# Optimization experiments

Measured on AMD Instinct MI355X. Metric: run time of the kernel, lower is better.

## Reference

```python
import jax, jax.numpy as jnp
import numpy as np


def setup_inputs() -> dict:
    key = jax.random.key(0)
    k0, k1, k2, k3 = jax.random.split(key, 4)
    B, S, D, F, E = 2, 2048, 1024, 4096, 8
    hidden_states = jax.random.normal(k0, (B, S, D), dtype=jnp.float32)
    Wr = jax.random.normal(k1, (E, D), dtype=jnp.float32) * 0.02   # router Linear weight [E, D]
    W1 = jax.random.normal(k2, (E, D, F), dtype=jnp.float32) * 0.02  # expert w1 (transposed torch layout)
    W2 = jax.random.normal(k3, (E, F, D), dtype=jnp.float32) * 0.02  # expert w2
    return {"hidden_states": hidden_states, "Wr": Wr, "W1": W1, "W2": W2, "top_k": 2}


def reference(hidden_states, Wr, W1, W2, top_k):
    # hidden_states: [B, S, D]; Wr: [E, D]; W1: [E, D, F]; W2: [E, F, D]
    E = Wr.shape[0]
    dt = hidden_states.dtype

    # Router: logits -> top-k expert indices. NOTE: the original module computes
    # softmax routing weights over the top-k logits but never applies them in the
    # combine step, so the output is an UNWEIGHTED sum over selected experts.
    router_logits = jnp.einsum('bsd,ed->bse', hidden_states, Wr)
    _, topk_idx = jax.lax.top_k(router_logits, top_k)            # [B, S, K]

    # mask[b,s,e] = 1 if expert e is in token (b,s)'s top-k (indices are distinct)
    mask = (jax.nn.one_hot(topk_idx, E, dtype=dt).sum(axis=-2) > 0).astype(dt)  # [B, S, E]

    # Dense per-expert FFN (SiLU MLP, no bias, dropout=identity in eval):
    h = jax.nn.silu(jnp.einsum('bsd,edf->bsef', hidden_states, W1))  # [B, S, E, F]
    y = jnp.einsum('bsef,efd->bsed', h, W2)                          # [B, S, E, D]

    # Combine: unweighted sum over selected experts (faithful to source)
    return jnp.einsum('bsed,bse->bsd', y, mask)
```

## Files before the change

kernel.cpp:

```cpp
#include <hip/hip_runtime.h>
#include <hip/hip_bf16.h>
#include <stdint.h>

#define TOKENS 4096
#define DDIM 1024
#define FDIM 4096
#define NEXP 8
#define BM 128
#define BN 128
#define BK2 32

typedef __attribute__((ext_vector_type(4))) float f32x4;
typedef __attribute__((ext_vector_type(8))) short short8;

__device__ __forceinline__ unsigned short f2bf(float f) {
    union { float f; uint32_t u; } v; v.f = f;
    uint32_t u = v.u;
    return (unsigned short)((u + 0x7fff + ((u >> 16) & 1)) >> 16);
}

#define BARRIER() asm volatile("s_barrier" ::: "memory")
#define WAIT_VM0() asm volatile("s_waitcnt vmcnt(0)" ::: "memory")
#define WAIT_VM4() asm volatile("s_waitcnt vmcnt(4)" ::: "memory")
#define WAIT_LGKM0() asm volatile("s_waitcnt lgkmcnt(0)" ::: "memory")
#define GLDS(SRC, DST) __builtin_amdgcn_global_load_lds( \
    (const __attribute__((address_space(1))) void*)(SRC), \
    (__attribute__((address_space(3))) void*)(DST), 16, 0, 0)

__device__ __forceinline__ short8 dsr(uint32_t addr) {
    short8 d;
    asm volatile("ds_read_b128 %0, %1" : "=v"(d) : "v"(addr));
    return d;
}

__global__ __launch_bounds__(256) void cvt_x(const float* __restrict__ x,
                                             unsigned short* __restrict__ xb, int n) {
    int i = (blockIdx.x * 256 + threadIdx.x) * 8;
    if (i >= n) return;
    float4 a = *(const float4*)(x + i);
    float4 b = *(const float4*)(x + i + 4);
    short8 o;
    o[0] = f2bf(a.x); o[1] = f2bf(a.y); o[2] = f2bf(a.z); o[3] = f2bf(a.w);
    o[4] = f2bf(b.x); o[5] = f2bf(b.y); o[6] = f2bf(b.z); o[7] = f2bf(b.w);
    *(short8*)(xb + i) = o;
}

__global__ __launch_bounds__(256) void transpose_cvt(const float* __restrict__ in,
                                                     unsigned short* __restrict__ out,
                                                     int R, int C) {
    __shared__ float tile[32][33];
    int e = blockIdx.z;
    int r0 = blockIdx.y * 32, c0 = blockIdx.x * 32;
    const float* src = in + (size_t)e * R * C;
    unsigned short* dst = out + (size_t)e * R * C;
    int t = threadIdx.x;
    int rr = t >> 3;
    int cc = (t & 7) * 4;
    float4 v = *(const float4*)(src + (size_t)(r0 + rr) * C + c0 + cc);
    tile[rr][cc + 0] = v.x; tile[rr][cc + 1] = v.y;
    tile[rr][cc + 2] = v.z; tile[rr][cc + 3] = v.w;
    __syncthreads();
    int oc = rr;
    int orr = cc;
    ushort4 o;
    o.x = f2bf(tile[orr + 0][oc]);
    o.y = f2bf(tile[orr + 1][oc]);
    o.z = f2bf(tile[orr + 2][oc]);
    o.w = f2bf(tile[orr + 3][oc]);
    *(ushort4*)(dst + (size_t)(c0 + oc) * R + r0 + orr) = o;
}

__global__ __launch_bounds__(256) void router(const float* __restrict__ x,
                                              const float* __restrict__ wr,
                                              int* __restrict__ cnt,
                                              int* __restrict__ list) {
    __shared__ float wl[NEXP * DDIM];
    int t = threadIdx.x;
    for (int i = t; i < NEXP * DDIM; i += 256) wl[i] = wr[i];
    __syncthreads();
    int tok = blockIdx.x * 4 + (t >> 6);
    int lane = t & 63;
    float acc[NEXP];
#pragma unroll
    for (int e = 0; e < NEXP; e++) acc[e] = 0.f;
    const float* xr = x + (size_t)tok * DDIM;
    for (int d = lane; d < DDIM; d += 64) {
        float xv = xr[d];
#pragma unroll
        for (int e = 0; e < NEXP; e++) acc[e] += xv * wl[e * DDIM + d];
    }
#pragma unroll
    for (int e = 0; e < NEXP; e++) {
#pragma unroll
        for (int off = 32; off; off >>= 1) acc[e] += __shfl_xor(acc[e], off);
    }
    if (lane == 0) {
        int e1 = 0; float v1 = acc[0];
        for (int e = 1; e < NEXP; e++) if (acc[e] > v1) { v1 = acc[e]; e1 = e; }
        int e2 = -1; float v2 = -1e30f;
        for (int e = 0; e < NEXP; e++) if (e != e1 && acc[e] > v2) { v2 = acc[e]; e2 = e; }
        int p1 = atomicAdd(&cnt[e1], 1);
        list[e1 * TOKENS + p1] = tok;
        int p2 = atomicAdd(&cnt[e2], 1);
        list[e2 * TOKENS + p2] = tok;
    }
}

__global__ void setup(const int* __restrict__ cnt, int* __restrict__ off,
                      int* __restrict__ wbA, int* __restrict__ wbB,
                      int* __restrict__ qctr) {
    if (threadIdx.x == 0) {
        int s = 0, ta = 0, tb = 0;
        for (int e = 0; e < NEXP; e++) {
            off[e] = s; s += cnt[e];
            wbA[e] = ta; wbB[e] = tb;
            int ntm = (cnt[e] + BM - 1) / BM;
            ta += ntm * (FDIM / BN);
            tb += ntm * (DDIM / BN) * 2;
        }
        wbA[NEXP] = ta; wbB[NEXP] = tb;
        qctr[0] = 0; qctr[1] = 0;
    }
}

template <bool GATHER_A, bool SILU, int KSPLIT>
__global__ __launch_bounds__(256, 3) void gemm_moe8(
    const unsigned short* __restrict__ Abase,
    const unsigned short* __restrict__ Wt,
    const int* __restrict__ cnt, const int* __restrict__ off,
    const int* __restrict__ list,
    const int* __restrict__ wbase,
    int* __restrict__ qctr,
    unsigned short* __restrict__ Hout,
    float* __restrict__ Yout,
    int KD, int KLEN, int NW) {
    __shared__ alignas(16) unsigned short As[3][BM * BK2];
    __shared__ alignas(16) unsigned short Bs[3][BN * BK2];
    __shared__ int wsh;

    const int t = threadIdx.x;
    const int lane = t & 63;
    const int wid = t >> 6;
    const int wm = wid >> 1, wn = wid & 1;
    const int r16 = lane & 15, g = lane >> 4;
    const int total = wbase[NEXP];

    const uint32_t asB = (uint32_t)(uintptr_t)&As[0][0];
    const uint32_t bsB = (uint32_t)(uintptr_t)&Bs[0][0];
    uint32_t aAdr[4], bAdr[4];
#pragma unroll
    for (int mi = 0; mi < 4; mi++) {
        int row = wm * 64 + mi * 16 + r16;
        aAdr[mi] = asB + row * 64 + ((g ^ ((row >> 1) & 3)) << 4);
    }
#pragma unroll
    for (int nj = 0; nj < 4; nj++) {
        int row = wn * 64 + nj * 16 + r16;
        bAdr[nj] = bsB + row * 64 + ((g ^ ((row >> 1) & 3)) << 4);
    }

    for (;;) {
        if (t == 0) wsh = atomicAdd(qctr, 1);
        __syncthreads();
        int w = wsh;
        if (w >= total) break;

        int e = 0;
        while (e < NEXP - 1 && w >= wbase[e + 1]) e++;
        w -= wbase[e];
        const int n_e = cnt[e];
        const int ntm = (n_e + BM - 1) >> 7;
        int idx = w / ntm;
        const int mtile = w - idx * ntm;
        int kc = 0;
        if (KSPLIT == 2) { kc = idx & 1; idx >>= 1; }
        const int m0 = mtile * BM;
        const int n0 = idx * BN;
        const int base = off[e];
        const int k0 = kc * KLEN;

        const unsigned short* pA[2];
        const unsigned short* pB[2];
        int ldsOff[2];
#pragma unroll
        for (int i = 0; i < 2; i++) {
            int c = i * 256 + t;
            int row = c >> 2, p = c & 3;
            int cg = p ^ ((row >> 1) & 3);
            int arow = m0 + row; if (arow >= n_e) arow = n_e - 1;
            size_t grow = GATHER_A ? (size_t)list[e * TOKENS + arow] : (size_t)(base + arow);
            pA[i] = Abase + grow * (size_t)KD + k0 + (cg << 3);
            pB[i] = Wt + ((size_t)e * NW + n0 + row) * (size_t)KD + k0 + (cg << 3);
            ldsOff[i] = c * 16;
        }

        f32x4 acc[4][4];
#pragma unroll
        for (int i = 0; i < 4; i++)
#pragma unroll
            for (int j = 0; j < 4; j++) acc[i][j] = f32x4{0.f, 0.f, 0.f, 0.f};

#pragma unroll
        for (int s = 0; s < 2; ++s) {
#pragma unroll
            for (int i = 0; i < 2; i++) { GLDS(pA[i], (char*)As[s] + ldsOff[i]); pA[i] += BK2; }
#pragma unroll
            for (int i = 0; i < 2; i++) { GLDS(pB[i], (char*)Bs[s] + ldsOff[i]); pB[i] += BK2; }
        }
        WAIT_VM4();
        BARRIER();

        uint32_t o0 = 0, o1 = 8192, o2 = 16384;

        const int NT = KLEN / BK2;
        for (int tk = 0; tk < NT; ++tk) {
            if (tk + 2 < NT) {
#pragma unroll
                for (int i = 0; i < 2; i++) { GLDS(pA[i], (char*)As[0] + o2 + ldsOff[i]); pA[i] += BK2; }
#pragma unroll
                for (int i = 0; i < 2; i++) { GLDS(pB[i], (char*)Bs[0] + o2 + ldsOff[i]); pB[i] += BK2; }
            }

            short8 a0 = dsr(aAdr[0] + o0);
            short8 a1 = dsr(aAdr[1] + o0);
            short8 a2 = dsr(aAdr[2] + o0);
            short8 a3 = dsr(aAdr[3] + o0);
            short8 b0 = dsr(bAdr[0] + o0);
            short8 b1 = dsr(bAdr[1] + o0);
            short8 b2 = dsr(bAdr[2] + o0);
            short8 b3 = dsr(bAdr[3] + o0);
            WAIT_LGKM0();
            __builtin_amdgcn_sched_barrier(0);

            __builtin_amdgcn_s_setprio(1);
            acc[0][0] = __builtin_amdgcn_mfma_f32_16x16x32_bf16(a0, b0, acc[0][0], 0, 0, 0);
            acc[0][1] = __builtin_amdgcn_mfma_f32_16x16x32_bf16(a0, b1, acc[0][1], 0, 0, 0);
            acc[0][2] = __builtin_amdgcn_mfma_f32_16x16x32_bf16(a0, b2, acc[0][2], 0, 0, 0);
            acc[0][3] = __builtin_amdgcn_mfma_f32_16x16x32_bf16(a0, b3, acc[0][3], 0, 0, 0);
            acc[1][0] = __builtin_amdgcn_mfma_f32_16x16x32_bf16(a1, b0, acc[1][0], 0, 0, 0);
            acc[1][1] = __builtin_amdgcn_mfma_f32_16x16x32_bf16(a1, b1, acc[1][1], 0, 0, 0);
            acc[1][2] = __builtin_amdgcn_mfma_f32_16x16x32_bf16(a1, b2, acc[1][2], 0, 0, 0);
            acc[1][3] = __builtin_amdgcn_mfma_f32_16x16x32_bf16(a1, b3, acc[1][3], 0, 0, 0);
            acc[2][0] = __builtin_amdgcn_mfma_f32_16x16x32_bf16(a2, b0, acc[2][0], 0, 0, 0);
            acc[2][1] = __builtin_amdgcn_mfma_f32_16x16x32_bf16(a2, b1, acc[2][1], 0, 0, 0);
            acc[2][2] = __builtin_amdgcn_mfma_f32_16x16x32_bf16(a2, b2, acc[2][2], 0, 0, 0);
            acc[2][3] = __builtin_amdgcn_mfma_f32_16x16x32_bf16(a2, b3, acc[2][3], 0, 0, 0);
            acc[3][0] = __builtin_amdgcn_mfma_f32_16x16x32_bf16(a3, b0, acc[3][0], 0, 0, 0);
            acc[3][1] = __builtin_amdgcn_mfma_f32_16x16x32_bf16(a3, b1, acc[3][1], 0, 0, 0);
            acc[3][2] = __builtin_amdgcn_mfma_f32_16x16x32_bf16(a3, b2, acc[3][2], 0, 0, 0);
            acc[3][3] = __builtin_amdgcn_mfma_f32_16x16x32_bf16(a3, b3, acc[3][3], 0, 0, 0);
            __builtin_amdgcn_s_setprio(0);

            if (tk + 1 < NT) {
                if (tk + 2 < NT) WAIT_VM4();
                else             WAIT_VM0();
                BARRIER();
            }
            uint32_t tmp = o0; o0 = o1; o1 = o2; o2 = tmp;
        }

#pragma unroll
        for (int mi = 0; mi < 4; ++mi) {
#pragma unroll
            for (int nj = 0; nj < 4; ++nj) {
#pragma unroll
                for (int qq = 0; qq < 4; ++qq) {
                    int lr = wm * 64 + mi * 16 + g * 4 + qq;
                    if (m0 + lr < n_e) {
                        int col = n0 + wn * 64 + nj * 16 + r16;
                        float v = acc[mi][nj][qq];
                        if (SILU) {
                            v = v / (1.f + __expf(-v));
                            Hout[(size_t)(base + m0 + lr) * NW + col] = f2bf(v);
                        } else {
                            int tok = list[e * TOKENS + m0 + lr];
                            atomicAdd(&Yout[(size_t)tok * NW + col], v);
                        }
                    }
                }
            }
        }
    }
}

extern "C" void kernel_launch(void* const* d_in, const int* in_sizes, int n_in,
                              void* d_out, int out_size, void* d_ws, size_t ws_size,
                              hipStream_t stream) {
    const float* X  = (const float*)d_in[0];
    const float* Wr = (const float*)d_in[1];
    const float* W1 = (const float*)d_in[2];
    const float* W2 = (const float*)d_in[3];
    float* Y = (float*)d_out;

    char* ws = (char*)d_ws;
    int* cnt  = (int*)(ws + 0);
    int* off  = (int*)(ws + 64);
    int* wbA  = (int*)(ws + 128);
    int* wbB  = (int*)(ws + 192);
    int* qctr = (int*)(ws + 256);
    int* list = (int*)(ws + 1024);
    unsigned short* Xb = (unsigned short*)(ws + (1ull << 20));
    unsigned short* WT = (unsigned short*)(ws + (16ull << 20));
    unsigned short* H  = (unsigned short*)(ws + (80ull << 20));

    hipMemsetAsync(d_out, 0, (size_t)out_size * sizeof(float), stream);
    hipMemsetAsync(cnt, 0, 32, stream);

    cvt_x<<<TOKENS * DDIM / (256 * 8), 256, 0, stream>>>(X, Xb, TOKENS * DDIM);
    router<<<TOKENS / 4, 256, 0, stream>>>(X, Wr, cnt, list);
    setup<<<1, 64, 0, stream>>>(cnt, off, wbA, wbB, qctr);

    transpose_cvt<<<dim3(FDIM / 32, DDIM / 32, NEXP), 256, 0, stream>>>(W1, WT, DDIM, FDIM);
    gemm_moe8<true, true, 1><<<768, 256, 0, stream>>>(
        Xb, WT, cnt, off, list, wbA, qctr + 0, H, nullptr, DDIM, DDIM, FDIM);

    transpose_cvt<<<dim3(DDIM / 32, FDIM / 32, NEXP), 256, 0, stream>>>(W2, WT, FDIM, DDIM);
    gemm_moe8<false, false, 2><<<768, 256, 0, stream>>>(
        H, WT, cnt, off, list, wbB, qctr + 1, nullptr, Y, FDIM, FDIM / 2, DDIM);
}
```

Baseline: 463.1 us.

## Partition persistent GEMM work queue per XCD with work stealing

Replaces the single global atomic work counter with eight per-XCD queues, each owning a contiguous slice of the tile range. Workgroups read their XCD id from a hardware register and pull from their own queue first, falling back to the other queues once it is drained. The goal is to keep neighbouring tiles, which share weight and activation panels, on the same XCD so its L2 is reused, and to spread atomic contention across eight counters. When its own queue is empty a workgroup may issue up to eight atomics before finding work, and the per-queue limits now have to be kept in step with the tile ordering.

New measurement: 1.227 ms. 165% more time.

```diff
diff --git a/kernel.cpp b/kernel.cpp
--- a/kernel.cpp
+++ b/kernel.cpp
@@ -108,7 +108,8 @@
 
 __global__ void setup(const int* __restrict__ cnt, int* __restrict__ off,
                       int* __restrict__ wbA, int* __restrict__ wbB,
-                      int* __restrict__ qctr) {
+                      int* __restrict__ qA, int* __restrict__ qlA,
+                      int* __restrict__ qB, int* __restrict__ qlB) {
     if (threadIdx.x == 0) {
         int s = 0, ta = 0, tb = 0;
         for (int e = 0; e < NEXP; e++) {
@@ -119,18 +120,23 @@
             tb += ntm * (DDIM / BN) * 2;
         }
         wbA[NEXP] = ta; wbB[NEXP] = tb;
-        qctr[0] = 0; qctr[1] = 0;
+        for (int x = 0; x < 8; x++) {
+            qA[x]  = (int)((long)ta * x / 8);
+            qlA[x] = (int)((long)ta * (x + 1) / 8);
+            qB[x]  = (int)((long)tb * x / 8);
+            qlB[x] = (int)((long)tb * (x + 1) / 8);
+        }
     }
 }
 
 template <bool GATHER_A, bool SILU, int KSPLIT>
-__global__ __launch_bounds__(256, 3) void gemm_moe8(
+__global__ __launch_bounds__(256, 3) void gemm_moe9(
     const unsigned short* __restrict__ Abase,
     const unsigned short* __restrict__ Wt,
     const int* __restrict__ cnt, const int* __restrict__ off,
     const int* __restrict__ list,
     const int* __restrict__ wbase,
-    int* __restrict__ qctr,
+    int* __restrict__ qctr, const int* __restrict__ qlim,
     unsigned short* __restrict__ Hout,
     float* __restrict__ Yout,
     int KD, int KLEN, int NW) {
@@ -143,7 +149,10 @@
     const int wid = t >> 6;
     const int wm = wid >> 1, wn = wid & 1;
     const int r16 = lane & 15, g = lane >> 4;
-    const int total = wbase[NEXP];
+
+    uint32_t xcd;
+    asm volatile("s_getreg_b32 %0, hwreg(HW_REG_XCC_ID)" : "=s"(xcd));
+    int myq = (int)(xcd & 7);
 
     const uint32_t asB = (uint32_t)(uintptr_t)&As[0][0];
     const uint32_t bsB = (uint32_t)(uintptr_t)&Bs[0][0];
@@ -160,10 +169,18 @@
     }
 
     for (;;) {
-        if (t == 0) wsh = atomicAdd(qctr, 1);
+        if (t == 0) {
+            int w = -1;
+            for (int k = 0; k < 8 && w < 0; k++) {
+                int q = (myq + k) & 7;
+                int cand = atomicAdd(&qctr[q], 1);
+                if (cand < qlim[q]) { w = cand; myq = q; }
+            }
+            wsh = w;
+        }
         __syncthreads();
         int w = wsh;
-        if (w >= total) break;
+        if (w < 0) break;
 
         int e = 0;
         while (e < NEXP - 1 && w >= wbase[e + 1]) e++;
@@ -297,7 +314,10 @@
     int* off  = (int*)(ws + 64);
     int* wbA  = (int*)(ws + 128);
     int* wbB  = (int*)(ws + 192);
-    int* qctr = (int*)(ws + 256);
+    int* qA   = (int*)(ws + 256);
+    int* qlA  = (int*)(ws + 288);
+    int* qB   = (int*)(ws + 320);
+    int* qlB  = (int*)(ws + 352);
     int* list = (int*)(ws + 1024);
     unsigned short* Xb = (unsigned short*)(ws + (1ull << 20));
     unsigned short* WT = (unsigned short*)(ws + (16ull << 20));
@@ -308,13 +328,13 @@
 
     cvt_x<<<TOKENS * DDIM / (256 * 8), 256, 0, stream>>>(X, Xb, TOKENS * DDIM);
     router<<<TOKENS / 4, 256, 0, stream>>>(X, Wr, cnt, list);
-    setup<<<1, 64, 0, stream>>>(cnt, off, wbA, wbB, qctr);
+    setup<<<1, 64, 0, stream>>>(cnt, off, wbA, wbB, qA, qlA, qB, qlB);
 
     transpose_cvt<<<dim3(FDIM / 32, DDIM / 32, NEXP), 256, 0, stream>>>(W1, WT, DDIM, FDIM);
-    gemm_moe8<true, true, 1><<<768, 256, 0, stream>>>(
-        Xb, WT, cnt, off, list, wbA, qctr + 0, H, nullptr, DDIM, DDIM, FDIM);
+    gemm_moe9<true, true, 1><<<768, 256, 0, stream>>>(
+        Xb, WT, cnt, off, list, wbA, qA, qlA, H, nullptr, DDIM, DDIM, FDIM);
 
     transpose_cvt<<<dim3(DDIM / 32, FDIM / 32, NEXP), 256, 0, stream>>>(W2, WT, FDIM, DDIM);
-    gemm_moe8<false, false, 2><<<768, 256, 0, stream>>>(
-        H, WT, cnt, off, list, wbB, qctr + 1, nullptr, Y, FDIM, FDIM / 2, DDIM);
-}
+    gemm_moe9<false, false, 2><<<768, 256, 0, stream>>>(
+        H, WT, cnt, off, list, wbB, qB, qlB, nullptr, Y, FDIM, FDIM / 2, DDIM);
+}
```

## Use 256x64 tiles with 8-wave blocks and 4-way K split in down-proj

Applied to the files above, without the earlier changes.

Moves the MoE GEMM tile from 128x128 with 4 waves to 256x64 with 8 waves (512 threads). Each wave now computes a 64x32 sub-tile, only half the waves load B, and the vmcnt waits are adjusted to match. The down-projection GEMM goes from a 2-way to a 4-way K split, which doubles the atomic output traffic but adds more work items for load balance. The aim is better latency hiding and occupancy, at the cost of fewer MFMAs per LDS read per wave.

Result: slower. 513.7 us (+10.9%).

```diff
diff --git a/kernel.cpp b/kernel.cpp
--- a/kernel.cpp
+++ b/kernel.cpp
@@ -6,8 +6,8 @@
 #define DDIM 1024
 #define FDIM 4096
 #define NEXP 8
-#define BM 128
-#define BN 128
+#define BM 256
+#define BN 64
 #define BK2 32
 
 typedef __attribute__((ext_vector_type(4))) float f32x4;
@@ -21,7 +21,8 @@
 
 #define BARRIER() asm volatile("s_barrier" ::: "memory")
 #define WAIT_VM0() asm volatile("s_waitcnt vmcnt(0)" ::: "memory")
-#define WAIT_VM4() asm volatile("s_waitcnt vmcnt(4)" ::: "memory")
+#define WAIT_VM2() asm volatile("s_waitcnt vmcnt(2)" ::: "memory")
+#define WAIT_VM3() asm volatile("s_waitcnt vmcnt(3)" ::: "memory")
 #define WAIT_LGKM0() asm volatile("s_waitcnt lgkmcnt(0)" ::: "memory")
 #define GLDS(SRC, DST) __builtin_amdgcn_global_load_lds( \
     (const __attribute__((address_space(1))) void*)(SRC), \
@@ -114,9 +115,9 @@
         for (int e = 0; e < NEXP; e++) {
             off[e] = s; s += cnt[e];
             wbA[e] = ta; wbB[e] = tb;
-            int ntm = (cnt[e] + BM - 1) / BM;
-            ta += ntm * (FDIM / BN);
-            tb += ntm * (DDIM / BN) * 2;
+            int ntm = (cnt[e] + BM - 1) >> 8;
+            ta += ntm * 64;
+            tb += ntm * 64;
         }
         wbA[NEXP] = ta; wbB[NEXP] = tb;
         qctr[0] = 0; qctr[1] = 0;
@@ -124,7 +125,7 @@
 }
 
 template <bool GATHER_A, bool SILU, int KSPLIT>
-__global__ __launch_bounds__(256, 3) void gemm_moe8(
+__global__ __launch_bounds__(512, 2) void gemm_moe10(
     const unsigned short* __restrict__ Abase,
     const unsigned short* __restrict__ Wt,
     const int* __restrict__ cnt, const int* __restrict__ off,
@@ -143,19 +144,20 @@
     const int wid = t >> 6;
     const int wm = wid >> 1, wn = wid & 1;
     const int r16 = lane & 15, g = lane >> 4;
+    const bool loadsB = (wid < 4);
     const int total = wbase[NEXP];
 
     const uint32_t asB = (uint32_t)(uintptr_t)&As[0][0];
     const uint32_t bsB = (uint32_t)(uintptr_t)&Bs[0][0];
-    uint32_t aAdr[4], bAdr[4];
+    uint32_t aAdr[4], bAdr[2];
 #pragma unroll
     for (int mi = 0; mi < 4; mi++) {
         int row = wm * 64 + mi * 16 + r16;
         aAdr[mi] = asB + row * 64 + ((g ^ ((row >> 1) & 3)) << 4);
     }
 #pragma unroll
-    for (int nj = 0; nj < 4; nj++) {
-        int row = wn * 64 + nj * 16 + r16;
+    for (int nj = 0; nj < 2; nj++) {
+        int row = wn * 32 + nj * 16 + r16;
         bAdr[nj] = bsB + row * 64 + ((g ^ ((row >> 1) & 3)) << 4);
     }
 
@@ -169,105 +171,102 @@
         while (e < NEXP - 1 && w >= wbase[e + 1]) e++;
         w -= wbase[e];
         const int n_e = cnt[e];
-        const int ntm = (n_e + BM - 1) >> 7;
-        int idx = w / ntm;
-        const int mtile = w - idx * ntm;
-        int kc = 0;
-        if (KSPLIT == 2) { kc = idx & 1; idx >>= 1; }
+        const int ntm = (n_e + BM - 1) >> 8;
+        int combined = w / ntm;
+        const int mtile = w - combined * ntm;
+        const int kc = combined & (KSPLIT - 1);
+        const int idx = combined / KSPLIT;
         const int m0 = mtile * BM;
         const int n0 = idx * BN;
         const int base = off[e];
         const int k0 = kc * KLEN;
 
         const unsigned short* pA[2];
-        const unsigned short* pB[2];
-        int ldsOff[2];
+        int ldsA[2];
 #pragma unroll
         for (int i = 0; i < 2; i++) {
-            int c = i * 256 + t;
+            int c = i * 512 + t;
             int row = c >> 2, p = c & 3;
             int cg = p ^ ((row >> 1) & 3);
             int arow = m0 + row; if (arow >= n_e) arow = n_e - 1;
             size_t grow = GATHER_A ? (size_t)list[e * TOKENS + arow] : (size_t)(base + arow);
             pA[i] = Abase + grow * (size_t)KD + k0 + (cg << 3);
-            pB[i] = Wt + ((size_t)e * NW + n0 + row) * (size_t)KD + k0 + (cg << 3);
-            ldsOff[i] = c * 16;
-        }
-
-        f32x4 acc[4][4];
+            ldsA[i] = c * 16;
+        }
+        const unsigned short* pB;
+        int ldsB;
+        {
+            int c = t & 255;
+            int row = c >> 2, p = c & 3;
+            int cg = p ^ ((row >> 1) & 3);
+            pB = Wt + ((size_t)e * NW + n0 + row) * (size_t)KD + k0 + (cg << 3);
+            ldsB = c * 16;
+        }
+
+        f32x4 acc[4][2];
 #pragma unroll
         for (int i = 0; i < 4; i++)
 #pragma unroll
-            for (int j = 0; j < 4; j++) acc[i][j] = f32x4{0.f, 0.f, 0.f, 0.f};
+            for (int j = 0; j < 2; j++) acc[i][j] = f32x4{0.f, 0.f, 0.f, 0.f};
 
 #pragma unroll
         for (int s = 0; s < 2; ++s) {
 #pragma unroll
-            for (int i = 0; i < 2; i++) { GLDS(pA[i], (char*)As[s] + ldsOff[i]); pA[i] += BK2; }
-#pragma unroll
-            for (int i = 0; i < 2; i++) { GLDS(pB[i], (char*)Bs[s] + ldsOff[i]); pB[i] += BK2; }
-        }
-        WAIT_VM4();
+            for (int i = 0; i < 2; i++) { GLDS(pA[i], (char*)As[s] + ldsA[i]); pA[i] += BK2; }
+            if (loadsB) { GLDS(pB, (char*)Bs[s] + ldsB); pB += BK2; }
+        }
+        if (loadsB) WAIT_VM3(); else WAIT_VM2();
         BARRIER();
 
-        uint32_t o0 = 0, o1 = 8192, o2 = 16384;
+        uint32_t uA0 = 0, uA1 = 16384, uA2 = 32768;
+        uint32_t uB0 = 0, uB1 = 4096, uB2 = 8192;
 
         const int NT = KLEN / BK2;
         for (int tk = 0; tk < NT; ++tk) {
             if (tk + 2 < NT) {
 #pragma unroll
-                for (int i = 0; i < 2; i++) { GLDS(pA[i], (char*)As[0] + o2 + ldsOff[i]); pA[i] += BK2; }
-#pragma unroll
-                for (int i = 0; i < 2; i++) { GLDS(pB[i], (char*)Bs[0] + o2 + ldsOff[i]); pB[i] += BK2; }
+                for (int i = 0; i < 2; i++) { GLDS(pA[i], (char*)As[0] + uA2 + ldsA[i]); pA[i] += BK2; }
+                if (loadsB) { GLDS(pB, (char*)Bs[0] + uB2 + ldsB); pB += BK2; }
             }
 
-            short8 a0 = dsr(aAdr[0] + o0);
-            short8 a1 = dsr(aAdr[1] + o0);
-            short8 a2 = dsr(aAdr[2] + o0);
-            short8 a3 = dsr(aAdr[3] + o0);
-            short8 b0 = dsr(bAdr[0] + o0);
-            short8 b1 = dsr(bAdr[1] + o0);
-            short8 b2 = dsr(bAdr[2] + o0);
-            short8 b3 = dsr(bAdr[3] + o0);
+            short8 a0 = dsr(aAdr[0] + uA0);
+            short8 a1 = dsr(aAdr[1] + uA0);
+            short8 a2 = dsr(aAdr[2] + uA0);
+            short8 a3 = dsr(aAdr[3] + uA0);
+            short8 b0 = dsr(bAdr[0] + uB0);
+            short8 b1 = dsr(bAdr[1] + uB0);
             WAIT_LGKM0();
             __builtin_amdgcn_sched_barrier(0);
 
             __builtin_amdgcn_s_setprio(1);
             acc[0][0] = __builtin_amdgcn_mfma_f32_16x16x32_bf16(a0, b0, acc[0][0], 0, 0, 0);
             acc[0][1] = __builtin_amdgcn_mfma_f32_16x16x32_bf16(a0, b1, acc[0][1], 0, 0, 0);
-            acc[0][2] = __builtin_amdgcn_mfma_f32_16x16x32_bf16(a0, b2, acc[0][2], 0, 0, 0);
-            acc[0][3] = __builtin_amdgcn_mfma_f32_16x16x32_bf16(a0, b3, acc[0][3], 0, 0, 0);
             acc[1][0] = __builtin_amdgcn_mfma_f32_16x16x32_bf16(a1, b0, acc[1][0], 0, 0, 0);
             acc[1][1] = __builtin_amdgcn_mfma_f32_16x16x32_bf16(a1, b1, acc[1][1], 0, 0, 0);
-            acc[1][2] = __builtin_amdgcn_mfma_f32_16x16x32_bf16(a1, b2, acc[1][2], 0, 0, 0);
-            acc[1][3] = __builtin_amdgcn_mfma_f32_16x16x32_bf16(a1, b3, acc[1][3], 0, 0, 0);
             acc[2][0] = __builtin_amdgcn_mfma_f32_16x16x32_bf16(a2, b0, acc[2][0], 0, 0, 0);
             acc[2][1] = __builtin_amdgcn_mfma_f32_16x16x32_bf16(a2, b1, acc[2][1], 0, 0, 0);
-            acc[2][2] = __builtin_amdgcn_mfma_f32_16x16x32_bf16(a2, b2, acc[2][2], 0, 0, 0);
-            acc[2][3] = __builtin_amdgcn_mfma_f32_16x16x32_bf16(a2, b3, acc[2][3], 0, 0, 0);
             acc[3][0] = __builtin_amdgcn_mfma_f32_16x16x32_bf16(a3, b0, acc[3][0], 0, 0, 0);
             acc[3][1] = __builtin_amdgcn_mfma_f32_16x16x32_bf16(a3, b1, acc[3][1], 0, 0, 0);
-            acc[3][2] = __builtin_amdgcn_mfma_f32_16x16x32_bf16(a3, b2, acc[3][2], 0, 0, 0);
-            acc[3][3] = __builtin_amdgcn_mfma_f32_16x16x32_bf16(a3, b3, acc[3][3], 0, 0, 0);
             __builtin_amdgcn_s_setprio(0);
 
             if (tk + 1 < NT) {
-                if (tk + 2 < NT) WAIT_VM4();
+                if (tk + 2 < NT) { if (loadsB) WAIT_VM3(); else WAIT_VM2(); }
                 else             WAIT_VM0();
                 BARRIER();
             }
-            uint32_t tmp = o0; o0 = o1; o1 = o2; o2 = tmp;
+            uint32_t ta_ = uA0; uA0 = uA1; uA1 = uA2; uA2 = ta_;
+            uint32_t tb_ = uB0; uB0 = uB1; uB1 = uB2; uB2 = tb_;
         }
 
 #pragma unroll
         for (int mi = 0; mi < 4; ++mi) {
 #pragma unroll
-            for (int nj = 0; nj < 4; ++nj) {
+            for (int nj = 0; nj < 2; ++nj) {
 #pragma unroll
                 for (int qq = 0; qq < 4; ++qq) {
                     int lr = wm * 64 + mi * 16 + g * 4 + qq;
                     if (m0 + lr < n_e) {
-                        int col = n0 + wn * 64 + nj * 16 + r16;
+                        int col = n0 + wn * 32 + nj * 16 + r16;
                         float v = acc[mi][nj][qq];
                         if (SILU) {
                             v = v / (1.f + __expf(-v));
@@ -311,10 +310,10 @@
     setup<<<1, 64, 0, stream>>>(cnt, off, wbA, wbB, qctr);
 
     transpose_cvt<<<dim3(FDIM / 32, DDIM / 32, NEXP), 256, 0, stream>>>(W1, WT, DDIM, FDIM);
-    gemm_moe8<true, true, 1><<<768, 256, 0, stream>>>(
+    gemm_moe10<true, true, 1><<<512, 512, 0, stream>>>(
         Xb, WT, cnt, off, list, wbA, qctr + 0, H, nullptr, DDIM, DDIM, FDIM);
 
     transpose_cvt<<<dim3(DDIM / 32, FDIM / 32, NEXP), 256, 0, stream>>>(W2, WT, FDIM, DDIM);
-    gemm_moe8<false, false, 2><<<768, 256, 0, stream>>>(
-        H, WT, cnt, off, list, wbB, qctr + 1, nullptr, Y, FDIM, FDIM / 2, DDIM);
-}
+    gemm_moe10<false, false, 4><<<512, 512, 0, stream>>>(
+        H, WT, cnt, off, list, wbB, qctr + 1, nullptr, Y, FDIM, FDIM / 4, DDIM);
+}
```

## Switch MoE GEMMs to double buffering, raise occupancy, split-K by four

Applied to the files above, without the earlier changes.

Cuts the LDS ring from three stages to two so four workgroups can be resident per CU (launch bounds 4, grid 1024 persistent blocks). The second GEMM's K dimension is now split into four chunks instead of two, which doubles the work items and the fp32 atomic adds into the output. The prefetch distance drops to one tile with a full vmcnt(0) wait each iteration. The aim is latency hiding through more resident waves rather than deeper per-block pipelining, at the cost of less in-block overlap and more atomic traffic.

After: 538.2 us. 1.16x slower.

```diff
diff --git a/kernel.cpp b/kernel.cpp
--- a/kernel.cpp
+++ b/kernel.cpp
@@ -21,7 +21,6 @@
 
 #define BARRIER() asm volatile("s_barrier" ::: "memory")
 #define WAIT_VM0() asm volatile("s_waitcnt vmcnt(0)" ::: "memory")
-#define WAIT_VM4() asm volatile("s_waitcnt vmcnt(4)" ::: "memory")
 #define WAIT_LGKM0() asm volatile("s_waitcnt lgkmcnt(0)" ::: "memory")
 #define GLDS(SRC, DST) __builtin_amdgcn_global_load_lds( \
     (const __attribute__((address_space(1))) void*)(SRC), \
@@ -116,7 +115,7 @@
             wbA[e] = ta; wbB[e] = tb;
             int ntm = (cnt[e] + BM - 1) / BM;
             ta += ntm * (FDIM / BN);
-            tb += ntm * (DDIM / BN) * 2;
+            tb += ntm * (DDIM / BN) * 4;
         }
         wbA[NEXP] = ta; wbB[NEXP] = tb;
         qctr[0] = 0; qctr[1] = 0;
@@ -124,7 +123,7 @@
 }
 
 template <bool GATHER_A, bool SILU, int KSPLIT>
-__global__ __launch_bounds__(256, 3) void gemm_moe8(
+__global__ __launch_bounds__(256, 4) void gemm_moe13(
     const unsigned short* __restrict__ Abase,
     const unsigned short* __restrict__ Wt,
     const int* __restrict__ cnt, const int* __restrict__ off,
@@ -134,8 +133,8 @@
     unsigned short* __restrict__ Hout,
     float* __restrict__ Yout,
     int KD, int KLEN, int NW) {
-    __shared__ alignas(16) unsigned short As[3][BM * BK2];
-    __shared__ alignas(16) unsigned short Bs[3][BN * BK2];
+    __shared__ alignas(16) unsigned short As[2][BM * BK2];
+    __shared__ alignas(16) unsigned short Bs[2][BN * BK2];
     __shared__ int wsh;
 
     const int t = threadIdx.x;
@@ -170,10 +169,10 @@
         w -= wbase[e];
         const int n_e = cnt[e];
         const int ntm = (n_e + BM - 1) >> 7;
-        int idx = w / ntm;
-        const int mtile = w - idx * ntm;
-        int kc = 0;
-        if (KSPLIT == 2) { kc = idx & 1; idx >>= 1; }
+        int combined = w / ntm;
+        const int mtile = w - combined * ntm;
+        const int kc = (KSPLIT > 1) ? (combined & (KSPLIT - 1)) : 0;
+        const int idx = (KSPLIT > 1) ? (combined / KSPLIT) : combined;
         const int m0 = mtile * BM;
         const int n0 = idx * BN;
         const int base = off[e];
@@ -201,24 +200,24 @@
             for (int j = 0; j < 4; j++) acc[i][j] = f32x4{0.f, 0.f, 0.f, 0.f};
 
 #pragma unroll
-        for (int s = 0; s < 2; ++s) {
-#pragma unroll
-            for (int i = 0; i < 2; i++) { GLDS(pA[i], (char*)As[s] + ldsOff[i]); pA[i] += BK2; }
-#pragma unroll
-            for (int i = 0; i < 2; i++) { GLDS(pB[i], (char*)Bs[s] + ldsOff[i]); pB[i] += BK2; }
-        }
-        WAIT_VM4();
+        for (int i = 0; i < 2; i++) { GLDS(pA[i], (char*)As[0] + ldsOff[i]); pA[i] += BK2; }
+#pragma unroll
+        for (int i = 0; i < 2; i++) { GLDS(pB[i], (char*)Bs[0] + ldsOff[i]); pB[i] += BK2; }
+        WAIT_VM0();
         BARRIER();
-
-        uint32_t o0 = 0, o1 = 8192, o2 = 16384;
 
         const int NT = KLEN / BK2;
         for (int tk = 0; tk < NT; ++tk) {
-            if (tk + 2 < NT) {
-#pragma unroll
-                for (int i = 0; i < 2; i++) { GLDS(pA[i], (char*)As[0] + o2 + ldsOff[i]); pA[i] += BK2; }
-#pragma unroll
-                for (int i = 0; i < 2; i++) { GLDS(pB[i], (char*)Bs[0] + o2 + ldsOff[i]); pB[i] += BK2; }
+            const int cur = tk & 1;
+            const uint32_t o0 = cur ? 8192u : 0u;
+
+            if (tk + 1 < NT) {
+                char* Ad = (char*)As[cur ^ 1];
+                char* Bd = (char*)Bs[cur ^ 1];
+#pragma unroll
+                for (int i = 0; i < 2; i++) { GLDS(pA[i], Ad + ldsOff[i]); pA[i] += BK2; }
+#pragma unroll
+                for (int i = 0; i < 2; i++) { GLDS(pB[i], Bd + ldsOff[i]); pB[i] += BK2; }
             }
 
             short8 a0 = dsr(aAdr[0] + o0);
@@ -252,11 +251,9 @@
             __builtin_amdgcn_s_setprio(0);
 
             if (tk + 1 < NT) {
-                if (tk + 2 < NT) WAIT_VM4();
-                else             WAIT_VM0();
+                WAIT_VM0();
                 BARRIER();
             }
-            uint32_t tmp = o0; o0 = o1; o1 = o2; o2 = tmp;
         }
 
 #pragma unroll
@@ -311,10 +308,10 @@
     setup<<<1, 64, 0, stream>>>(cnt, off, wbA, wbB, qctr);
 
     transpose_cvt<<<dim3(FDIM / 32, DDIM / 32, NEXP), 256, 0, stream>>>(W1, WT, DDIM, FDIM);
-    gemm_moe8<true, true, 1><<<768, 256, 0, stream>>>(
+    gemm_moe13<true, true, 1><<<1024, 256, 0, stream>>>(
         Xb, WT, cnt, off, list, wbA, qctr + 0, H, nullptr, DDIM, DDIM, FDIM);
 
     transpose_cvt<<<dim3(DDIM / 32, FDIM / 32, NEXP), 256, 0, stream>>>(W2, WT, FDIM, DDIM);
-    gemm_moe8<false, false, 2><<<768, 256, 0, stream>>>(
-        H, WT, cnt, off, list, wbB, qctr + 1, nullptr, Y, FDIM, FDIM / 2, DDIM);
-}
+    gemm_moe13<false, false, 4><<<1024, 256, 0, stream>>>(
+        H, WT, cnt, off, list, wbB, qctr + 1, nullptr, Y, FDIM, FDIM / 4, DDIM);
+}
```
